# Performance work log

Measured on AMD Instinct MI355X. Metric: run time of the kernel, lower is better.

The kernel has to match this reference:

```python
import jax, jax.numpy as jnp
from jax import lax
import numpy as np

# Config (matches init_kwargs)
V = 8           # num_variables
E = 256         # embed_dim
LAGS = 4
W = 64          # window_size
STEP = 16       # step_size
K = 512         # num_tokens (codebook size)
B = 32
S = 8256        # samples; (S - W) % STEP == 0 -> T = 512 windows
T = (S - W) // STEP
CONV_OUT = (W - LAGS) // LAGS + 1   # 16 positions after strided conv


def setup_inputs() -> dict:
    key = jax.random.key(0)
    ks = jax.random.split(key, 6)
    x = jax.random.normal(ks[0], (B, V, S), dtype=jnp.float32)
    conv_w = jax.random.normal(ks[1], (E, V, LAGS), dtype=jnp.float32) * 0.1
    conv_b = jax.random.normal(ks[2], (E,), dtype=jnp.float32) * 0.01
    lin_w = jax.random.normal(ks[3], (E, E * CONV_OUT), dtype=jnp.float32) * 0.02
    lin_b = jax.random.normal(ks[4], (E,), dtype=jnp.float32) * 0.01
    codebook = jax.random.normal(ks[5], (K, E), dtype=jnp.float32)
    return {"x": x, "conv_w": conv_w, "conv_b": conv_b,
            "lin_w": lin_w, "lin_b": lin_b, "codebook": codebook}


def _encode_windows(x, conv_w, conv_b, lin_w, lin_b):
    # Extract all sliding windows at once: starts [T], offsets [W] -> idx [T, W]
    starts = jnp.arange(T) * STEP
    idx = starts[:, None] + jnp.arange(W)[None, :]
    xw = x[:, :, idx]                         # [B, V, T, W]
    xw = xw.transpose(0, 2, 1, 3).reshape(B * T, V, W)  # batch all windows
    # TCN encoder: strided Conv1d(V->E, kernel=LAGS, stride=LAGS) + ReLU
    y = lax.conv_general_dilated(
        xw, conv_w, window_strides=(LAGS,), padding='VALID',
        dimension_numbers=('NCH', 'OIH', 'NCH'))   # [B*T, E, CONV_OUT]
    y = jax.nn.relu(y + conv_b[None, :, None])
    # Flatten + Linear -> embedding per window
    e = y.reshape(B * T, E * CONV_OUT) @ lin_w.T + lin_b  # [B*T, E]
    return e


def reference(x, conv_w, conv_b, lin_w, lin_b, codebook):
    e = _encode_windows(x, conv_w, conv_b, lin_w, lin_b)   # [B*T, E]
    # Vector quantization: nearest codebook entry by L2 distance
    d = (jnp.sum(e * e, axis=1, keepdims=True)
         - 2.0 * (e @ codebook.T)
         + jnp.sum(codebook * codebook, axis=1)[None, :])  # [B*T, K]
    idx = jnp.argmin(d, axis=1)                            # [B*T]
    q = codebook[idx]                                      # [B*T, E]
    # straight-through estimator (standard VQ forward value == q)
    out = e + lax.stop_gradient(q - e)
    return out.reshape(B, T, E)
```

## Files before the change

kernel.cpp:

```cpp
#include <hip/hip_runtime.h>

typedef _Float16 f16;
typedef _Float16 f16x4 __attribute__((ext_vector_type(4)));
typedef _Float16 f16x8 __attribute__((ext_vector_type(8)));
typedef float    f32x16 __attribute__((ext_vector_type(16)));

#define NB 32
#define TTOT 512
#define SSN 8256
#define PT 2064
#define EE 256
#define KCB 512

#define YB   ((size_t)NB*EE*PT*2)
#define LWB  ((size_t)EE*4096*2)
#define CBB  ((size_t)KCB*EE*2)
#define EBB  ((size_t)16384*EE*2)
#define OFF_Y0  ((size_t)0)
#define OFF_Y1  (YB)
#define OFF_LW0 (2*YB)
#define OFF_LW1 (2*YB + LWB)
#define OFF_CB0 (2*YB + 2*LWB)
#define OFF_CB1 (2*YB + 2*LWB + CBB)
#define OFF_HN  (2*YB + 2*LWB + 2*CBB)
#define OFF_E0  (OFF_HN + 4096)
#define OFF_E1  (OFF_E0 + EBB)
#define WS_NEED (OFF_E1 + EBB)

#define INV2048 4.8828125e-4f

struct h2 { f16 hi, lo; };
__device__ __forceinline__ h2 split2(float v) {
  h2 r;
  r.hi = (f16)v;
  r.lo = (f16)((v - (float)r.hi) * 2048.0f);
  return r;
}

__device__ __forceinline__ f16x8 ldsfrag(const f16* p) {
  union { f16x8 v8; f16x4 v4[2]; } u;
  u.v4[0] = *(const f16x4*)p;
  u.v4[1] = *(const f16x4*)(p + 4);
  return u.v8;
}

#define MFMA16(a,b,c) __builtin_amdgcn_mfma_f32_32x32x16_f16(a, b, c, 0, 0, 0)

__global__ __launch_bounds__(256, 2)
void k0_split(const float* __restrict__ lin_w, const float* __restrict__ cbk,
              f16* __restrict__ lwp0, f16* __restrict__ lwp1,
              f16* __restrict__ cbp0, f16* __restrict__ cbp1, float* __restrict__ hn)
{
  __shared__ float part[4][32];
  const int tid = threadIdx.x, bid = blockIdx.x;
  if (bid < 256) {
    const int eo = bid, nb = eo >> 5, lo = eo & 31;
    const int ep = tid;
    const float* src = lin_w + (size_t)eo * 4096 + ep * 16;
    float f[16];
    *(float4*)(f + 0)  = ((const float4*)src)[0];
    *(float4*)(f + 4)  = ((const float4*)src)[1];
    *(float4*)(f + 8)  = ((const float4*)src)[2];
    *(float4*)(f + 12) = ((const float4*)src)[3];
    union { f16x8 v; f16 e[8]; } a0, a1, b0, b1;
#pragma unroll
    for (int i = 0; i < 8; ++i) {
      { h2 s = split2(f[i]);     a0.e[i] = s.hi; a1.e[i] = s.lo; }
      { h2 s = split2(f[i + 8]); b0.e[i] = s.hi; b1.e[i] = s.lo; }
    }
    const size_t base = ((size_t)nb * 16384 + (size_t)ep * 64 + lo) * 8;
    *(f16x8*)(lwp0 + base)       = a0.v;
    *(f16x8*)(lwp0 + base + 256) = b0.v;
    *(f16x8*)(lwp1 + base)       = a1.v;
    *(f16x8*)(lwp1 + base + 256) = b1.v;
  } else {
    const int jb = bid - 256;
    const int lane = tid & 63, ksg = tid >> 6;
    const int hi = lane >> 5, lo = lane & 31;
    const int j = jb * 32 + lo;
    float s = 0.f;
#pragma unroll
    for (int kq = 0; kq < 4; ++kq) {
      const int ks = ksg * 4 + kq;
      const float* src = cbk + (size_t)j * 256 + ks * 16 + 8 * hi;
      float f[8];
      *(float4*)(f + 0) = ((const float4*)src)[0];
      *(float4*)(f + 4) = ((const float4*)src)[1];
      union { f16x8 v; f16 e[8]; } h0, h1;
#pragma unroll
      for (int i = 0; i < 8; ++i) {
        s = fmaf(f[i], f[i], s);
        h2 t = split2(f[i]); h0.e[i] = t.hi; h1.e[i] = t.lo;
      }
      const size_t base = ((size_t)jb * 1024 + (size_t)ks * 64 + lane) * 8;
      *(f16x8*)(cbp0 + base) = h0.v;
      *(f16x8*)(cbp1 + base) = h1.v;
    }
    s += __shfl_xor(s, 32, 64);
    if (lane < 32) part[ksg][lane] = s;
    __syncthreads();
    if (tid < 32)
      hn[jb * 32 + tid] = 0.5f * (part[0][tid] + part[1][tid] + part[2][tid] + part[3][tid]);
  }
}

__global__ __launch_bounds__(256, 2)
void k1_conv(const float* __restrict__ x, const float* __restrict__ cw,
             const float* __restrict__ cb, f16* __restrict__ y0, f16* __restrict__ y1)
{
  const int bid = blockIdx.x;
  const int b = bid / 18, rem = bid % 18;
  const int eq = rem / 9, ptile = rem % 9;
  const int p = ptile * 256 + threadIdx.x;
  const bool valid = p < PT;
  const int pc = valid ? p : (PT - 1);
  float4 xv[8];
#pragma unroll
  for (int v = 0; v < 8; ++v)
    xv[v] = *(const float4*)(x + ((size_t)b * 8 + v) * SSN + 4 * pc);
  const int e0 = eq * 128;
  float4 wc[8], wn[8];
#pragma unroll
  for (int v = 0; v < 8; ++v) wc[v] = *(const float4*)(cw + (size_t)e0 * 32 + v * 4);
  for (int ep = e0; ep < e0 + 128; ++ep) {
    const int epn = (ep + 1 < e0 + 128) ? ep + 1 : ep;
#pragma unroll
    for (int v = 0; v < 8; ++v) wn[v] = *(const float4*)(cw + (size_t)epn * 32 + v * 4);
    float a = cb[ep];
#pragma unroll
    for (int v = 0; v < 8; ++v) {
      a = fmaf(xv[v].x, wc[v].x, a);
      a = fmaf(xv[v].y, wc[v].y, a);
      a = fmaf(xv[v].z, wc[v].z, a);
      a = fmaf(xv[v].w, wc[v].w, a);
    }
    a = fmaxf(a, 0.f);
    if (valid) {
      const h2 s = split2(a);
      const size_t o = ((size_t)b * EE + ep) * PT + p;
      y0[o] = s.hi; y1[o] = s.lo;
    }
#pragma unroll
    for (int v = 0; v < 8; ++v) wc[v] = wn[v];
  }
}

__global__ __launch_bounds__(256, 2)
void k2_linear(const f16* __restrict__ yh0, const f16* __restrict__ yh1,
               const f16* __restrict__ lwp0, const f16* __restrict__ lwp1,
               const float* __restrict__ lin_b,
               f16* __restrict__ eh0, f16* __restrict__ eh1)
{
  __shared__ __align__(16) f16 ysh[2][2][4][272];
  const int tid = threadIdx.x;
  const int sw = (blockIdx.x & 7) * 64 + (blockIdx.x >> 3);
  const int nh = sw >> 8, mt = sw & 255;
  const int b = mt >> 3;
  const int p0 = (mt & 7) * 256;
  const int lane = tid & 63, wv = tid >> 6;
  const int m = wv >> 1, nq = wv & 1;
  const int hi = lane >> 5, lo = lane & 31;

  const f16* pBp[2][2];
#pragma unroll
  for (int n = 0; n < 2; ++n) {
    const int nb = nh * 4 + nq * 2 + n;
    pBp[n][0] = lwp0 + ((size_t)nb * 16384 + lane) * 8;
    pBp[n][1] = lwp1 + ((size_t)nb * 16384 + lane) * 8;
  }
  const int aoff = 4 * (m * 32 + lo) + 8 * hi;

  const int sr = tid >> 5, sc = tid & 31;
  const int slimb = sr >> 2, ske = sr & 3;
  const bool has2 = sc < 2;
  const f16* ysrc = (slimb ? yh1 : yh0);

  f32x16 accH[2], accL[2];
#pragma unroll
  for (int n = 0; n < 2; ++n)
#pragma unroll
    for (int r = 0; r < 16; ++r) { accH[n][r] = 0.f; accL[n][r] = 0.f; }

  f16x8 bf[4][2][2];
#pragma unroll
  for (int d = 0; d < 4; ++d)
#pragma unroll
    for (int n = 0; n < 2; ++n) {
      bf[d][n][0] = *(const f16x8*)(pBp[n][0] + (size_t)d * 512);
      bf[d][n][1] = *(const f16x8*)(pBp[n][1] + (size_t)d * 512);
    }

  {
    const f16* src = ysrc + ((size_t)(b * EE + ske) * PT + p0) + sc * 8;
    const float4 sA = *(const float4*)src;
    float4 sB{};
    if (has2) sB = *(const float4*)(src + 256);
    f16* dst = &ysh[0][slimb][ske][sc * 8];
    *(float4*)dst = sA;
    if (has2) *(float4*)(dst + 256) = sB;
  }
  __syncthreads();

  for (int ss = 0; ss < 64; ++ss) {
    const int cur = ss & 1;
    const int ssn = (ss < 63) ? ss + 1 : 63;
    const f16* src = ysrc + ((size_t)(b * EE + ssn * 4 + ske) * PT + p0) + sc * 8;
    const float4 sA = *(const float4*)src;
    float4 sB{};
    if (has2) sB = *(const float4*)(src + 256);

    const f16* ab0 = &ysh[cur][0][0][0] + aoff;
    f16x8 a0 = ldsfrag(ab0);
    f16x8 a1 = ldsfrag(ab0 + 4 * 272);

#pragma unroll
    for (int ke = 0; ke < 4; ++ke) {
      f16x8 a0n, a1n;
      if (ke < 3) {
        const f16* abn = &ysh[cur][0][ke + 1][0] + aoff;
        a0n = ldsfrag(abn);
        a1n = ldsfrag(abn + 4 * 272);
      }
#pragma unroll
      for (int n = 0; n < 2; ++n) {
        accH[n] = MFMA16(a0, bf[ke][n][0], accH[n]);
        accL[n] = MFMA16(a0, bf[ke][n][1], accL[n]);
        accL[n] = MFMA16(a1, bf[ke][n][0], accL[n]);
      }
      {
        const int epn = ss * 4 + ke + 4;
        const size_t off = (size_t)((epn < 256) ? epn : 255) * 512;
#pragma unroll
        for (int n = 0; n < 2; ++n) {
          bf[ke][n][0] = *(const f16x8*)(pBp[n][0] + off);
          bf[ke][n][1] = *(const f16x8*)(pBp[n][1] + off);
        }
      }
      if (ke < 3) { a0 = a0n; a1 = a1n; }
    }

    {
      f16* dst = &ysh[cur ^ 1][slimb][ske][sc * 8];
      *(float4*)dst = sA;
      if (has2) *(float4*)(dst + 256) = sB;
    }
    __syncthreads();
  }

#pragma unroll
  for (int n = 0; n < 2; ++n) {
    const int eo = nh * 128 + (nq * 2 + n) * 32 + lo;
    const float lb = lin_b[eo];
#pragma unroll
    for (int r = 0; r < 16; ++r) {
      const int wloc = m * 32 + (r & 3) + 8 * (r >> 2) + 4 * hi;
      const float v = accH[n][r] + accL[n][r] * INV2048 + lb;
      const h2 s = split2(v);
      const size_t o = (size_t)(mt * 64 + wloc) * EE + eo;
      eh0[o] = s.hi; eh1[o] = s.lo;
    }
  }
}

__global__ __launch_bounds__(512, 1)
void k3_dist(const f16* __restrict__ eh0, const f16* __restrict__ eh1,
             const f16* __restrict__ cbp0, const f16* __restrict__ cbp1,
             const float* __restrict__ hn, const float* __restrict__ cbk,
             float* __restrict__ out)
{
  __shared__ __align__(16) f16 esh[2][64][136];
  __shared__ float scs[4][64];
  __shared__ int   scj[4][64];
  __shared__ int   bestj[64];
  const int tid = threadIdx.x;
  const int w0 = blockIdx.x * 64;
  const int lane = tid & 63, wv = tid >> 6;
  const int m = wv & 1, jg = wv >> 1;
  const int hi = lane >> 5, lo = lane & 31;

  const f16* pBp[4][2];
  float hnv[4];
#pragma unroll
  for (int q = 0; q < 4; ++q) {
    const int jb = jg * 4 + q;
    pBp[q][0] = cbp0 + ((size_t)jb * 1024 + lane) * 8;
    pBp[q][1] = cbp1 + ((size_t)jb * 1024 + lane) * 8;
    hnv[q] = hn[jb * 32 + lo];
  }
  f32x16 accH[4], accL[4];
#pragma unroll
  for (int q = 0; q < 4; ++q)
#pragma unroll
    for (int r = 0; r < 16; ++r) { accH[q][r] = 0.f; accL[q][r] = 0.f; }

  const int ar = m * 32 + lo;
  f16x8 BA[4][2], BB[4][2];
#pragma unroll
  for (int q = 0; q < 4; ++q) {
    BA[q][0] = *(const f16x8*)(pBp[q][0]);
    BA[q][1] = *(const f16x8*)(pBp[q][1]);
  }

  for (int kh = 0; kh < 2; ++kh) {
    if (kh) __syncthreads();
    {
      const int r = tid >> 3, c8 = tid & 7;
      const f16* s0 = eh0 + (size_t)(w0 + r) * EE + kh * 128;
      const f16* s1 = eh1 + (size_t)(w0 + r) * EE + kh * 128;
#pragma unroll
      for (int i = 0; i < 2; ++i) {
        const int c = (c8 * 2 + i) * 8;
        *(float4*)&esh[0][r][c] = *(const float4*)(s0 + c);
        *(float4*)&esh[1][r][c] = *(const float4*)(s1 + c);
      }
    }
    __syncthreads();
#pragma unroll
    for (int ksl = 0; ksl < 8; ++ksl) {
      const int ks = kh * 8 + ksl;
      const int ksn = (ks < 15) ? ks + 1 : 15;
      const f16x8 a0 = *(const f16x8*)(&esh[0][ar][0] + ksl * 16 + 8 * hi);
      const f16x8 a1 = *(const f16x8*)(&esh[1][ar][0] + ksl * 16 + 8 * hi);
      if ((ks & 1) == 0) {
#pragma unroll
        for (int q = 0; q < 4; ++q) {
          BB[q][0] = *(const f16x8*)(pBp[q][0] + (size_t)ksn * 512);
          BB[q][1] = *(const f16x8*)(pBp[q][1] + (size_t)ksn * 512);
        }
#pragma unroll
        for (int q = 0; q < 4; ++q) {
          accH[q] = MFMA16(a0, BA[q][0], accH[q]);
          accL[q] = MFMA16(a0, BA[q][1], accL[q]);
          accL[q] = MFMA16(a1, BA[q][0], accL[q]);
        }
      } else {
#pragma unroll
        for (int q = 0; q < 4; ++q) {
          BA[q][0] = *(const f16x8*)(pBp[q][0] + (size_t)ksn * 512);
          BA[q][1] = *(const f16x8*)(pBp[q][1] + (size_t)ksn * 512);
        }
#pragma unroll
        for (int q = 0; q < 4; ++q) {
          accH[q] = MFMA16(a0, BB[q][0], accH[q]);
          accL[q] = MFMA16(a0, BB[q][1], accL[q]);
          accL[q] = MFMA16(a1, BB[q][0], accL[q]);
        }
      }
    }
  }

#pragma unroll
  for (int r = 0; r < 16; ++r) {
    float bs = accH[0][r] + accL[0][r] * INV2048 - hnv[0];
    int   bj = (jg * 4 + 0) * 32 + lo;
#pragma unroll
    for (int q = 1; q < 4; ++q) {
      const float s = accH[q][r] + accL[q][r] * INV2048 - hnv[q];
      const int   j = (jg * 4 + q) * 32 + lo;
      if (s > bs) { bs = s; bj = j; }
    }
#pragma unroll
    for (int d = 1; d < 32; d <<= 1) {
      const float os = __shfl_xor(bs, d, 64);
      const int   oj = __shfl_xor(bj, d, 64);
      if (os > bs || (os == bs && oj < bj)) { bs = os; bj = oj; }
    }
    if (lo == 0) {
      const int wloc = m * 32 + (r & 3) + 8 * (r >> 2) + 4 * hi;
      scs[jg][wloc] = bs; scj[jg][wloc] = bj;
    }
  }
  __syncthreads();
  if (tid < 64) {
    float bs = scs[0][tid]; int bj = scj[0][tid];
#pragma unroll
    for (int g = 1; g < 4; ++g) {
      const float s = scs[g][tid]; const int j = scj[g][tid];
      if (s > bs || (s == bs && j < bj)) { bs = s; bj = j; }
    }
    bestj[tid] = bj;
  }
  __syncthreads();
  {
    const int rr = tid >> 6;
    const int c4 = (tid & 63) * 4;
#pragma unroll
    for (int pass = 0; pass < 8; ++pass) {
      const int r = pass * 8 + rr;
      const int jb = bestj[r];
      const float4 v = *(const float4*)(cbk + (size_t)jb * EE + c4);
      *(float4*)(out + (size_t)(w0 + r) * EE + c4) = v;
    }
  }
}

#define V 8
#define LAGS 4
#define WIN 64
#define STEP 16
#define CONV_OUT 16
#define WPB 16
#define TPB 256
#define NWORD 19
#define YSTRIDE 80
#define XSPAN 304
#define FOFF_YS   0
#define FOFF_XS   10240
#define FOFF_ES   10240
#define FOFF_SC   0
#define FOFF_SI   4096
#define FOFF_PS   8192
#define FOFF_PI   8448
#define FOFF_IW   8704
#define SMEM_FLOATS 14336

__device__ __forceinline__ float f4get(const float4& v, int i) {
  return i == 0 ? v.x : (i == 1 ? v.y : (i == 2 ? v.z : v.w));
}

__device__ __forceinline__ float conv_one(const float* xs, int p, const float4* cw, float cb0) {
  float a = cb0;
#pragma unroll
  for (int v = 0; v < V; ++v) {
    const float4 xv = *(const float4*)(xs + v * XSPAN + 4 * p);
    a = fmaf(xv.x, cw[v].x, a);
    a = fmaf(xv.y, cw[v].y, a);
    a = fmaf(xv.z, cw[v].z, a);
    a = fmaf(xv.w, cw[v].w, a);
  }
  return fmaxf(a, 0.0f);
}

__global__ __launch_bounds__(TPB, 2)
void tok_fused(const float* __restrict__ x, const float* __restrict__ conv_w,
               const float* __restrict__ conv_b, const float* __restrict__ lin_w,
               const float* __restrict__ lin_b, const float* __restrict__ cbk,
               float* __restrict__ out)
{
  __shared__ float smem[SMEM_FLOATS];
  float* ys = smem + FOFF_YS;
  float* xs = smem + FOFF_XS;
  float* es = smem + FOFF_ES;
  float* sc = smem + FOFF_SC;
  int*   si = (int*)(smem + FOFF_SI);
  float* ps = smem + FOFF_PS;
  int*   pi = (int*)(smem + FOFF_PI);
  int*   iw = (int*)(smem + FOFF_IW);
  const int tid = threadIdx.x;
  const int b   = blockIdx.x >> 5;
  const int t0  = (blockIdx.x & 31) * WPB;
  const float* xb = x + (size_t)b * V * SSN + (size_t)t0 * STEP;
#pragma unroll
  for (int v = 0; v < V; ++v)
    for (int j = tid; j < XSPAN; j += TPB)
      xs[v * XSPAN + j] = xb[(size_t)v * SSN + j];
  double accd[WPB];
#pragma unroll
  for (int w = 0; w < WPB; ++w) accd[w] = 0.0;
  for (int half = 0; half < 2; ++half) {
    __syncthreads();
    {
      const int ep  = half * 128 + (tid >> 1);
      const int row = ep & 127;
      float4 cw[V];
      const float4* cwp = (const float4*)(conv_w + (size_t)ep * (V * LAGS));
#pragma unroll
      for (int v = 0; v < V; ++v) cw[v] = cwp[v];
      const float cb0 = conv_b[ep];
      const int c0 = (tid & 1) ? 10 : 0;
      const int c1 = (tid & 1) ? NWORD : 10;
      for (int c = c0; c < c1; ++c) {
        const int p = 4 * c;
        float r0 = conv_one(xs, p + 0, cw, cb0);
        float r1 = conv_one(xs, p + 1, cw, cb0);
        float r2 = conv_one(xs, p + 2, cw, cb0);
        float r3 = conv_one(xs, p + 3, cw, cb0);
        *(float4*)(ys + row * YSTRIDE + 4 * c) = make_float4(r0, r1, r2, r3);
      }
    }
    __syncthreads();
    const float* lwbase = lin_w + (size_t)tid * (EE * CONV_OUT) + half * (128 * CONV_OUT);
    float4 nA, nB, nC, nD;
    {
      const float4* p4 = (const float4*)(lwbase);
      nA = p4[0]; nB = p4[1]; nC = p4[2]; nD = p4[3];
    }
    for (int er = 0; er < 128; ++er) {
      const float4 lA = nA, lB = nB, lC = nC, lD = nD;
      const int ern = (er + 1) & 127;
      {
        const float4* p4 = (const float4*)(lwbase + ern * CONV_OUT);
        nA = p4[0]; nB = p4[1]; nC = p4[2]; nD = p4[3];
      }
      float4 yr[NWORD];
      const float4* yp = (const float4*)(ys + er * YSTRIDE);
#pragma unroll
      for (int q = 0; q < NWORD; ++q) yr[q] = yp[q];
      float it[WPB];
#pragma unroll
      for (int w = 0; w < WPB; ++w) it[w] = 0.0f;
#pragma unroll
      for (int o = 0; o < CONV_OUT; ++o) {
        const float lw_o = f4get(o < 4 ? lA : (o < 8 ? lB : (o < 12 ? lC : lD)), o & 3);
#pragma unroll
        for (int w = 0; w < WPB; ++w) {
          const int p = 4 * w + o;
          it[w] = fmaf(lw_o, f4get(yr[p >> 2], p & 3), it[w]);
        }
      }
#pragma unroll
      for (int w = 0; w < WPB; ++w) accd[w] += (double)it[w];
    }
  }
#pragma unroll
  for (int w = 0; w < WPB; ++w)
    es[w * EE + tid] = (float)accd[w] + lin_b[tid];
  __syncthreads();
  float s_best[WPB];
  int   i_best[WPB];
#pragma unroll
  for (int jj = 0; jj < 2; ++jj) {
    const int j = tid + jj * 256;
    const float4* cbp = (const float4*)(cbk + (size_t)j * EE);
    double sdd[WPB];
    float  sd32[WPB];
#pragma unroll
    for (int w = 0; w < WPB; ++w) { sdd[w] = 0.0; sd32[w] = 0.f; }
    double ndd = 0.0;
    float  nd32 = 0.f;
    float4 c4n = cbp[0];
    for (int i16 = 0; i16 < 4; ++i16) {
      for (int i4i = 0; i4i < 16; ++i4i) {
        const int i4 = i16 * 16 + i4i;
        const float4 c4 = c4n;
        c4n = cbp[(i4 + 1 <= 63) ? (i4 + 1) : 63];
        nd32 = fmaf(c4.x, c4.x, nd32);
        nd32 = fmaf(c4.y, c4.y, nd32);
        nd32 = fmaf(c4.z, c4.z, nd32);
        nd32 = fmaf(c4.w, c4.w, nd32);
#pragma unroll
        for (int w = 0; w < WPB; ++w) {
          const float4 e4 = *(const float4*)(es + w * EE + i4 * 4);
          sd32[w] = fmaf(c4.x, e4.x, sd32[w]);
          sd32[w] = fmaf(c4.y, e4.y, sd32[w]);
          sd32[w] = fmaf(c4.z, e4.z, sd32[w]);
          sd32[w] = fmaf(c4.w, e4.w, sd32[w]);
        }
      }
#pragma unroll
      for (int w = 0; w < WPB; ++w) { sdd[w] += (double)sd32[w]; sd32[w] = 0.f; }
      ndd += (double)nd32; nd32 = 0.f;
    }
#pragma unroll
    for (int w = 0; w < WPB; ++w) {
      const float s = (float)(sdd[w] - 0.5 * ndd);
      if (jj == 0) { s_best[w] = s; i_best[w] = j; }
      else if (s > s_best[w]) { s_best[w] = s; i_best[w] = j; }
    }
  }
#pragma unroll
  for (int w = 0; w < WPB; ++w) {
    sc[w * EE + tid] = s_best[w];
    si[w * EE + tid] = i_best[w];
  }
  __syncthreads();
  {
    const int w = tid >> 4, seg = tid & 15;
    float mm = -INFINITY; int mi = 0x7fffffff;
    for (int t = seg * 16; t < seg * 16 + 16; ++t) {
      const float s = sc[w * EE + t];
      const int   jx = si[w * EE + t];
      if (s > mm || (s == mm && jx < mi)) { mm = s; mi = jx; }
    }
    ps[w * 16 + seg] = mm; pi[w * 16 + seg] = mi;
  }
  __syncthreads();
  if (tid < WPB) {
    const int w = tid;
    float mm = -INFINITY; int mi = 0x7fffffff;
    for (int t = 0; t < 16; ++t) {
      const float s = ps[w * 16 + t];
      const int   jx = pi[w * 16 + t];
      if (s > mm || (s == mm && jx < mi)) { mm = s; mi = jx; }
    }
    iw[w] = mi;
  }
  __syncthreads();
  const size_t outb = ((size_t)b * TTOT + t0) * EE;
#pragma unroll
  for (int w = 0; w < WPB; ++w)
    out[outb + (size_t)w * EE + tid] = cbk[(size_t)iw[w] * EE + tid];
}

extern "C" void kernel_launch(void* const* d_in, const int* in_sizes, int n_in,
                              void* d_out, int out_size, void* d_ws, size_t ws_size,
                              hipStream_t stream) {
  const float* x      = (const float*)d_in[0];
  const float* conv_w = (const float*)d_in[1];
  const float* conv_b = (const float*)d_in[2];
  const float* lin_w  = (const float*)d_in[3];
  const float* lin_b  = (const float*)d_in[4];
  const float* cbk    = (const float*)d_in[5];
  float* out = (float*)d_out;

  if (ws_size < WS_NEED) {
    tok_fused<<<dim3(32 * 32), dim3(TPB), 0, stream>>>(x, conv_w, conv_b, lin_w, lin_b, cbk, out);
    return;
  }
  char* ws = (char*)d_ws;
  f16*   y0  = (f16*)(ws + OFF_Y0);
  f16*   y1  = (f16*)(ws + OFF_Y1);
  f16*   lwp0 = (f16*)(ws + OFF_LW0);
  f16*   lwp1 = (f16*)(ws + OFF_LW1);
  f16*   cbp0 = (f16*)(ws + OFF_CB0);
  f16*   cbp1 = (f16*)(ws + OFF_CB1);
  float* hn  = (float*)(ws + OFF_HN);
  f16*   e0  = (f16*)(ws + OFF_E0);
  f16*   e1  = (f16*)(ws + OFF_E1);

  k0_split<<<272, 256, 0, stream>>>(lin_w, cbk, lwp0, lwp1, cbp0, cbp1, hn);
  k1_conv <<<576, 256, 0, stream>>>(x, conv_w, conv_b, y0, y1);
  k2_linear<<<512, 256, 0, stream>>>(y0, y1, lwp0, lwp1, lin_b, e0, e1);
  k3_dist <<<256, 512, 0, stream>>>(e0, e1, cbp0, cbp1, hn, cbk, out);
}
```

Measured before the change: 195.6 us.

## Stage linear weights in LDS with larger M tile; merge split and conv kernels

k2_linear now runs 512-thread blocks that each cover 128 windows instead of 64. The hi/lo weight fragments are staged through a double-buffered LDS tile shared by all waves, where before every wave streamed them from global memory itself. This halves weight traffic and removes per-wave redundant loads, at the cost of more LDS, fewer blocks (256) and extra LDS reads per MFMA. Separately, the weight/codebook split kernel and the conv kernel are merged into one launch to save a kernel boundary.

```diff
diff --git a/kernel.cpp b/kernel.cpp
--- a/kernel.cpp
+++ b/kernel.cpp
@@ -47,133 +47,134 @@
 #define MFMA16(a,b,c) __builtin_amdgcn_mfma_f32_32x32x16_f16(a, b, c, 0, 0, 0)
 
 __global__ __launch_bounds__(256, 2)
-void k0_split(const float* __restrict__ lin_w, const float* __restrict__ cbk,
-              f16* __restrict__ lwp0, f16* __restrict__ lwp1,
-              f16* __restrict__ cbp0, f16* __restrict__ cbp1, float* __restrict__ hn)
+void k01(const float* __restrict__ lin_w, const float* __restrict__ cbk,
+         f16* __restrict__ lwp0, f16* __restrict__ lwp1,
+         f16* __restrict__ cbp0, f16* __restrict__ cbp1, float* __restrict__ hn,
+         const float* __restrict__ x, const float* __restrict__ cw,
+         const float* __restrict__ cb, f16* __restrict__ y0, f16* __restrict__ y1)
 {
   __shared__ float part[4][32];
-  const int tid = threadIdx.x, bid = blockIdx.x;
-  if (bid < 256) {
-    const int eo = bid, nb = eo >> 5, lo = eo & 31;
-    const int ep = tid;
-    const float* src = lin_w + (size_t)eo * 4096 + ep * 16;
-    float f[16];
-    *(float4*)(f + 0)  = ((const float4*)src)[0];
-    *(float4*)(f + 4)  = ((const float4*)src)[1];
-    *(float4*)(f + 8)  = ((const float4*)src)[2];
-    *(float4*)(f + 12) = ((const float4*)src)[3];
-    union { f16x8 v; f16 e[8]; } a0, a1, b0, b1;
-#pragma unroll
-    for (int i = 0; i < 8; ++i) {
-      { h2 s = split2(f[i]);     a0.e[i] = s.hi; a1.e[i] = s.lo; }
-      { h2 s = split2(f[i + 8]); b0.e[i] = s.hi; b1.e[i] = s.lo; }
-    }
-    const size_t base = ((size_t)nb * 16384 + (size_t)ep * 64 + lo) * 8;
-    *(f16x8*)(lwp0 + base)       = a0.v;
-    *(f16x8*)(lwp0 + base + 256) = b0.v;
-    *(f16x8*)(lwp1 + base)       = a1.v;
-    *(f16x8*)(lwp1 + base + 256) = b1.v;
+  const int tid = threadIdx.x;
+  const int bix = blockIdx.x;
+  if (bix < 272) {
+    const int bid = bix;
+    if (bid < 256) {
+      const int eo = bid, nb = eo >> 5, lo = eo & 31;
+      const int ep = tid;
+      const float* src = lin_w + (size_t)eo * 4096 + ep * 16;
+      float f[16];
+      *(float4*)(f + 0)  = ((const float4*)src)[0];
+      *(float4*)(f + 4)  = ((const float4*)src)[1];
+      *(float4*)(f + 8)  = ((const float4*)src)[2];
+      *(float4*)(f + 12) = ((const float4*)src)[3];
+      union { f16x8 v; f16 e[8]; } a0, a1, b0, b1;
+#pragma unroll
+      for (int i = 0; i < 8; ++i) {
+        { h2 s = split2(f[i]);     a0.e[i] = s.hi; a1.e[i] = s.lo; }
+        { h2 s = split2(f[i + 8]); b0.e[i] = s.hi; b1.e[i] = s.lo; }
+      }
+      const size_t base = ((size_t)nb * 16384 + (size_t)ep * 64 + lo) * 8;
+      *(f16x8*)(lwp0 + base)       = a0.v;
+      *(f16x8*)(lwp0 + base + 256) = b0.v;
+      *(f16x8*)(lwp1 + base)       = a1.v;
+      *(f16x8*)(lwp1 + base + 256) = b1.v;
+    } else {
+      const int jb = bid - 256;
+      const int lane = tid & 63, ksg = tid >> 6;
+      const int hi = lane >> 5, lo = lane & 31;
+      const int j = jb * 32 + lo;
+      float s = 0.f;
+#pragma unroll
+      for (int kq = 0; kq < 4; ++kq) {
+        const int ks = ksg * 4 + kq;
+        const float* src = cbk + (size_t)j * 256 + ks * 16 + 8 * hi;
+        float f[8];
+        *(float4*)(f + 0) = ((const float4*)src)[0];
+        *(float4*)(f + 4) = ((const float4*)src)[1];
+        union { f16x8 v; f16 e[8]; } h0, h1;
+#pragma unroll
+        for (int i = 0; i < 8; ++i) {
+          s = fmaf(f[i], f[i], s);
+          h2 t = split2(f[i]); h0.e[i] = t.hi; h1.e[i] = t.lo;
+        }
+        const size_t base = ((size_t)jb * 1024 + (size_t)ks * 64 + lane) * 8;
+        *(f16x8*)(cbp0 + base) = h0.v;
+        *(f16x8*)(cbp1 + base) = h1.v;
+      }
+      s += __shfl_xor(s, 32, 64);
+      if (lane < 32) part[ksg][lane] = s;
+      __syncthreads();
+      if (tid < 32)
+        hn[jb * 32 + tid] = 0.5f * (part[0][tid] + part[1][tid] + part[2][tid] + part[3][tid]);
+    }
   } else {
-    const int jb = bid - 256;
-    const int lane = tid & 63, ksg = tid >> 6;
-    const int hi = lane >> 5, lo = lane & 31;
-    const int j = jb * 32 + lo;
-    float s = 0.f;
-#pragma unroll
-    for (int kq = 0; kq < 4; ++kq) {
-      const int ks = ksg * 4 + kq;
-      const float* src = cbk + (size_t)j * 256 + ks * 16 + 8 * hi;
-      float f[8];
-      *(float4*)(f + 0) = ((const float4*)src)[0];
-      *(float4*)(f + 4) = ((const float4*)src)[1];
-      union { f16x8 v; f16 e[8]; } h0, h1;
-#pragma unroll
-      for (int i = 0; i < 8; ++i) {
-        s = fmaf(f[i], f[i], s);
-        h2 t = split2(f[i]); h0.e[i] = t.hi; h1.e[i] = t.lo;
-      }
-      const size_t base = ((size_t)jb * 1024 + (size_t)ks * 64 + lane) * 8;
-      *(f16x8*)(cbp0 + base) = h0.v;
-      *(f16x8*)(cbp1 + base) = h1.v;
-    }
-    s += __shfl_xor(s, 32, 64);
-    if (lane < 32) part[ksg][lane] = s;
-    __syncthreads();
-    if (tid < 32)
-      hn[jb * 32 + tid] = 0.5f * (part[0][tid] + part[1][tid] + part[2][tid] + part[3][tid]);
-  }
-}
-
-__global__ __launch_bounds__(256, 2)
-void k1_conv(const float* __restrict__ x, const float* __restrict__ cw,
-             const float* __restrict__ cb, f16* __restrict__ y0, f16* __restrict__ y1)
-{
-  const int bid = blockIdx.x;
-  const int b = bid / 18, rem = bid % 18;
-  const int eq = rem / 9, ptile = rem % 9;
-  const int p = ptile * 256 + threadIdx.x;
-  const bool valid = p < PT;
-  const int pc = valid ? p : (PT - 1);
-  float4 xv[8];
-#pragma unroll
-  for (int v = 0; v < 8; ++v)
-    xv[v] = *(const float4*)(x + ((size_t)b * 8 + v) * SSN + 4 * pc);
-  const int e0 = eq * 128;
-  float4 wc[8], wn[8];
-#pragma unroll
-  for (int v = 0; v < 8; ++v) wc[v] = *(const float4*)(cw + (size_t)e0 * 32 + v * 4);
-  for (int ep = e0; ep < e0 + 128; ++ep) {
-    const int epn = (ep + 1 < e0 + 128) ? ep + 1 : ep;
-#pragma unroll
-    for (int v = 0; v < 8; ++v) wn[v] = *(const float4*)(cw + (size_t)epn * 32 + v * 4);
-    float a = cb[ep];
-#pragma unroll
-    for (int v = 0; v < 8; ++v) {
-      a = fmaf(xv[v].x, wc[v].x, a);
-      a = fmaf(xv[v].y, wc[v].y, a);
-      a = fmaf(xv[v].z, wc[v].z, a);
-      a = fmaf(xv[v].w, wc[v].w, a);
-    }
-    a = fmaxf(a, 0.f);
-    if (valid) {
-      const h2 s = split2(a);
-      const size_t o = ((size_t)b * EE + ep) * PT + p;
-      y0[o] = s.hi; y1[o] = s.lo;
-    }
-#pragma unroll
-    for (int v = 0; v < 8; ++v) wc[v] = wn[v];
-  }
-}
-
-__global__ __launch_bounds__(256, 2)
+    const int bid = bix - 272;
+    const int b = bid / 18, rem = bid % 18;
+    const int eq = rem / 9, ptile = rem % 9;
+    const int p = ptile * 256 + tid;
+    const bool valid = p < PT;
+    const int pc = valid ? p : (PT - 1);
+    float4 xv[8];
+#pragma unroll
+    for (int v = 0; v < 8; ++v)
+      xv[v] = *(const float4*)(x + ((size_t)b * 8 + v) * SSN + 4 * pc);
+    const int e0 = eq * 128;
+    float4 wc[8], wn[8];
+#pragma unroll
+    for (int v = 0; v < 8; ++v) wc[v] = *(const float4*)(cw + (size_t)e0 * 32 + v * 4);
+    for (int ep = e0; ep < e0 + 128; ++ep) {
+      const int epn = (ep + 1 < e0 + 128) ? ep + 1 : ep;
+#pragma unroll
+      for (int v = 0; v < 8; ++v) wn[v] = *(const float4*)(cw + (size_t)epn * 32 + v * 4);
+      float a = cb[ep];
+#pragma unroll
+      for (int v = 0; v < 8; ++v) {
+        a = fmaf(xv[v].x, wc[v].x, a);
+        a = fmaf(xv[v].y, wc[v].y, a);
+        a = fmaf(xv[v].z, wc[v].z, a);
+        a = fmaf(xv[v].w, wc[v].w, a);
+      }
+      a = fmaxf(a, 0.f);
+      if (valid) {
+        const h2 s = split2(a);
+        const size_t o = ((size_t)b * EE + ep) * PT + p;
+        y0[o] = s.hi; y1[o] = s.lo;
+      }
+#pragma unroll
+      for (int v = 0; v < 8; ++v) wc[v] = wn[v];
+    }
+  }
+}
+
+__global__ __launch_bounds__(512, 1)
 void k2_linear(const f16* __restrict__ yh0, const f16* __restrict__ yh1,
                const f16* __restrict__ lwp0, const f16* __restrict__ lwp1,
                const float* __restrict__ lin_b,
                f16* __restrict__ eh0, f16* __restrict__ eh1)
 {
-  __shared__ __align__(16) f16 ysh[2][2][4][272];
+  __shared__ __align__(16) f16 ysh[2][2][4][528];
+  __shared__ __align__(16) f16 bsh[2][4][4][2][512];
   const int tid = threadIdx.x;
-  const int sw = (blockIdx.x & 7) * 64 + (blockIdx.x >> 3);
-  const int nh = sw >> 8, mt = sw & 255;
-  const int b = mt >> 3;
-  const int p0 = (mt & 7) * 256;
+  const int sw = (blockIdx.x & 7) * 32 + (blockIdx.x >> 3);
+  const int nh = sw >> 7, mt = sw & 127;
+  const int b = mt >> 2;
+  const int p0 = (mt & 3) * 512;
   const int lane = tid & 63, wv = tid >> 6;
   const int m = wv >> 1, nq = wv & 1;
   const int hi = lane >> 5, lo = lane & 31;
-
-  const f16* pBp[2][2];
-#pragma unroll
-  for (int n = 0; n < 2; ++n) {
-    const int nb = nh * 4 + nq * 2 + n;
-    pBp[n][0] = lwp0 + ((size_t)nb * 16384 + lane) * 8;
-    pBp[n][1] = lwp1 + ((size_t)nb * 16384 + lane) * 8;
-  }
   const int aoff = 4 * (m * 32 + lo) + 8 * hi;
 
-  const int sr = tid >> 5, sc = tid & 31;
-  const int slimb = sr >> 2, ske = sr & 3;
-  const bool has2 = sc < 2;
-  const f16* ysrc = (slimb ? yh1 : yh0);
+  const int bke = wv >> 1;
+  const int bnb0 = (wv & 1) * 2;
+  const f16* bs[2][2];
+#pragma unroll
+  for (int j = 0; j < 2; ++j) {
+    bs[j][0] = lwp0 + ((size_t)(nh * 4 + bnb0 + j) * 256) * 512 + lane * 8;
+    bs[j][1] = lwp1 + ((size_t)(nh * 4 + bnb0 + j) * 256) * 512 + lane * 8;
+  }
+  const int ylimb = wv >> 2, yke = wv & 3;
+  const f16* ysrcp = ylimb ? yh1 : yh0;
+  const size_t ybase0 = ((size_t)b * EE + yke) * PT + p0 + lane * 8;
 
   f32x16 accH[2], accL[2];
 #pragma unroll
@@ -181,68 +182,56 @@
 #pragma unroll
     for (int r = 0; r < 16; ++r) { accH[n][r] = 0.f; accL[n][r] = 0.f; }
 
-  f16x8 bf[4][2][2];
-#pragma unroll
-  for (int d = 0; d < 4; ++d)
-#pragma unroll
-    for (int n = 0; n < 2; ++n) {
-      bf[d][n][0] = *(const f16x8*)(pBp[n][0] + (size_t)d * 512);
-      bf[d][n][1] = *(const f16x8*)(pBp[n][1] + (size_t)d * 512);
-    }
-
   {
-    const f16* src = ysrc + ((size_t)(b * EE + ske) * PT + p0) + sc * 8;
-    const float4 sA = *(const float4*)src;
-    float4 sB{};
-    if (has2) sB = *(const float4*)(src + 256);
-    f16* dst = &ysh[0][slimb][ske][sc * 8];
-    *(float4*)dst = sA;
-    if (has2) *(float4*)(dst + 256) = sB;
+    const size_t epo = (size_t)bke * 512;
+    float4 br[4];
+#pragma unroll
+    for (int i = 0; i < 4; ++i) br[i] = *(const float4*)(bs[i >> 1][i & 1] + epo);
+    const float4 ya = *(const float4*)(ysrcp + ybase0);
+    float4 yb{};
+    if (lane < 2) yb = *(const float4*)(ysrcp + ybase0 + 512);
+#pragma unroll
+    for (int i = 0; i < 4; ++i)
+      *(float4*)&bsh[0][bke][bnb0 + (i >> 1)][i & 1][lane * 8] = br[i];
+    f16* yd = &ysh[0][ylimb][yke][lane * 8];
+    *(float4*)yd = ya;
+    if (lane < 2) *(float4*)(yd + 512) = yb;
   }
   __syncthreads();
 
   for (int ss = 0; ss < 64; ++ss) {
     const int cur = ss & 1;
     const int ssn = (ss < 63) ? ss + 1 : 63;
-    const f16* src = ysrc + ((size_t)(b * EE + ssn * 4 + ske) * PT + p0) + sc * 8;
-    const float4 sA = *(const float4*)src;
-    float4 sB{};
-    if (has2) sB = *(const float4*)(src + 256);
-
-    const f16* ab0 = &ysh[cur][0][0][0] + aoff;
-    f16x8 a0 = ldsfrag(ab0);
-    f16x8 a1 = ldsfrag(ab0 + 4 * 272);
+    const size_t epo = (size_t)(ssn * 4 + bke) * 512;
+    float4 br[4];
+#pragma unroll
+    for (int i = 0; i < 4; ++i) br[i] = *(const float4*)(bs[i >> 1][i & 1] + epo);
+    const size_t yb0 = ybase0 + (size_t)ssn * 4 * PT;
+    const float4 ya = *(const float4*)(ysrcp + yb0);
+    float4 yb{};
+    if (lane < 2) yb = *(const float4*)(ysrcp + yb0 + 512);
 
 #pragma unroll
     for (int ke = 0; ke < 4; ++ke) {
-      f16x8 a0n, a1n;
-      if (ke < 3) {
-        const f16* abn = &ysh[cur][0][ke + 1][0] + aoff;
-        a0n = ldsfrag(abn);
-        a1n = ldsfrag(abn + 4 * 272);
-      }
+      const f16x8 a0 = ldsfrag(&ysh[cur][0][ke][aoff]);
+      const f16x8 a1 = ldsfrag(&ysh[cur][1][ke][aoff]);
 #pragma unroll
       for (int n = 0; n < 2; ++n) {
-        accH[n] = MFMA16(a0, bf[ke][n][0], accH[n]);
-        accL[n] = MFMA16(a0, bf[ke][n][1], accL[n]);
-        accL[n] = MFMA16(a1, bf[ke][n][0], accL[n]);
-      }
-      {
-        const int epn = ss * 4 + ke + 4;
-        const size_t off = (size_t)((epn < 256) ? epn : 255) * 512;
-#pragma unroll
-        for (int n = 0; n < 2; ++n) {
-          bf[ke][n][0] = *(const f16x8*)(pBp[n][0] + off);
-          bf[ke][n][1] = *(const f16x8*)(pBp[n][1] + off);
-        }
-      }
-      if (ke < 3) { a0 = a0n; a1 = a1n; }
-    }
-
+        const f16x8 b0 = *(const f16x8*)&bsh[cur][ke][nq * 2 + n][0][lane * 8];
+        const f16x8 b1 = *(const f16x8*)&bsh[cur][ke][nq * 2 + n][1][lane * 8];
+        accH[n] = MFMA16(a0, b0, accH[n]);
+        accL[n] = MFMA16(a0, b1, accL[n]);
+        accL[n] = MFMA16(a1, b0, accL[n]);
+      }
+    }
     {
-      f16* dst = &ysh[cur ^ 1][slimb][ske][sc * 8];
-      *(float4*)dst = sA;
-      if (has2) *(float4*)(dst + 256) = sB;
+      const int nxt = cur ^ 1;
+#pragma unroll
+      for (int i = 0; i < 4; ++i)
+        *(float4*)&bsh[nxt][bke][bnb0 + (i >> 1)][i & 1][lane * 8] = br[i];
+      f16* yd = &ysh[nxt][ylimb][yke][lane * 8];
+      *(float4*)yd = ya;
+      if (lane < 2) *(float4*)(yd + 512) = yb;
     }
     __syncthreads();
   }
@@ -256,7 +245,7 @@
       const int wloc = m * 32 + (r & 3) + 8 * (r >> 2) + 4 * hi;
       const float v = accH[n][r] + accL[n][r] * INV2048 + lb;
       const h2 s = split2(v);
-      const size_t o = (size_t)(mt * 64 + wloc) * EE + eo;
+      const size_t o = (size_t)(mt * 128 + wloc) * EE + eo;
       eh0[o] = s.hi; eh1[o] = s.lo;
     }
   }
@@ -608,18 +597,18 @@
     return;
   }
   char* ws = (char*)d_ws;
-  f16*   y0  = (f16*)(ws + OFF_Y0);
-  f16*   y1  = (f16*)(ws + OFF_Y1);
+  f16*   y0   = (f16*)(ws + OFF_Y0);
+  f16*   y1   = (f16*)(ws + OFF_Y1);
   f16*   lwp0 = (f16*)(ws + OFF_LW0);
   f16*   lwp1 = (f16*)(ws + OFF_LW1);
   f16*   cbp0 = (f16*)(ws + OFF_CB0);
   f16*   cbp1 = (f16*)(ws + OFF_CB1);
-  float* hn  = (float*)(ws + OFF_HN);
-  f16*   e0  = (f16*)(ws + OFF_E0);
-  f16*   e1  = (f16*)(ws + OFF_E1);
-
-  k0_split<<<272, 256, 0, stream>>>(lin_w, cbk, lwp0, lwp1, cbp0, cbp1, hn);
-  k1_conv <<<576, 256, 0, stream>>>(x, conv_w, conv_b, y0, y1);
-  k2_linear<<<512, 256, 0, stream>>>(y0, y1, lwp0, lwp1, lin_b, e0, e1);
+  float* hn   = (float*)(ws + OFF_HN);
+  f16*   e0   = (f16*)(ws + OFF_E0);
+  f16*   e1   = (f16*)(ws + OFF_E1);
+
+  k01<<<848, 256, 0, stream>>>(lin_w, cbk, lwp0, lwp1, cbp0, cbp1, hn,
+                               x, conv_w, conv_b, y0, y1);
+  k2_linear<<<256, 512, 0, stream>>>(y0, y1, lwp0, lwp1, lin_b, e0, e1);
   k3_dist <<<256, 512, 0, stream>>>(e0, e1, cbp0, cbp1, hn, cbk, out);
 }
```

Result: faster. 185.3 us (-5.3%).
